# Kernel optimization log

Measured on AMD Instinct MI355X. Metric: run time of the kernel, lower is better.

## Reference

```python
import jax, jax.numpy as jnp
import numpy as np


def _conv1x1_relu(x, W, b):
    # x: (B, Cin, N, k), W: (Cout, Cin), b: (Cout,) -> (B, Cout, N, k)
    return jax.nn.relu(jnp.einsum('bcnk,oc->bonk', x, W) + b[None, :, None, None])


def _knn_idx(pc, k):
    # pc: (B, C, N). Mirrors torch: dis_mat = -||pi - pj||^2, topk (largest) -> nearest.
    G = jnp.einsum('bcn,bcm->bnm', pc, pc)            # (B, N, N)
    sq = jnp.sum(pc * pc, axis=1)                      # (B, N)
    neg_dist = 2.0 * G - sq[:, :, None] - sq[:, None, :]
    _, idx = jax.lax.top_k(neg_dist, k)                # (B, N, k) int32
    return idx


def _group_points(x, idx):
    # x: (B, C, N), idx: (B, N, k) -> (B, C, N, k); out[b,c,n,j] = x[b,c,idx[b,n,j]]
    B, C, N = x.shape
    k = idx.shape[-1]
    idx2 = jnp.broadcast_to(idx.reshape(B, 1, N * k), (B, C, N * k))
    return jnp.take_along_axis(x, idx2, axis=2).reshape(B, C, N, k)


def setup_inputs() -> dict:
    key = jax.random.key(0)
    ks = jax.random.split(key, 8)
    B, N, C, O, K = 8, 4096, 64, 64, 16
    s = 0.05
    return {
        'xyz': jax.random.normal(ks[0], (B, 3, N), dtype=jnp.float32),
        'fea': jax.random.normal(ks[1], (B, C, N), dtype=jnp.float32),
        'Wg1': jax.random.normal(ks[2], (O, 10), dtype=jnp.float32) * s,
        'bg1': jnp.zeros((O,), dtype=jnp.float32),
        'Wg2': jax.random.normal(ks[3], (O, O), dtype=jnp.float32) * s,
        'bg2': jnp.zeros((O,), dtype=jnp.float32),
        'Wf1': jax.random.normal(ks[4], (O, 2 * C), dtype=jnp.float32) * s,
        'bf1': jnp.zeros((O,), dtype=jnp.float32),
        'Wf2': jax.random.normal(ks[5], (O, O), dtype=jnp.float32) * s,
        'bf2': jnp.zeros((O,), dtype=jnp.float32),
        'Wf3': jax.random.normal(ks[6], (O, O), dtype=jnp.float32) * s,
        'bf3': jnp.zeros((O,), dtype=jnp.float32),
        'k': 16,
    }


def reference(xyz, fea, Wg1, bg1, Wg2, bg2, Wf1, bf1, Wf2, bf2, Wf3, bf3, k):
    idx = _knn_idx(fea, k)                             # (B, N, k)

    # get_edge_point: (B, 10, N, k)
    xyz_knn = _group_points(xyz, idx)                  # (B, 3, N, k)
    xyz_c = jnp.broadcast_to(xyz[:, :, :, None], xyz_knn.shape)
    xyz_r = xyz_c - xyz_knn
    xyz_d = jnp.sqrt(jnp.sum(xyz_r * xyz_r, axis=1, keepdims=True))
    geo = jnp.concatenate([xyz_d, xyz_c, xyz_knn, xyz_r], axis=1)

    # get_edge_feature: (B, 2C, N, k)
    fea_knn = _group_points(fea, idx)
    fea_c = jnp.broadcast_to(fea[:, :, :, None], fea_knn.shape)
    edge = jnp.concatenate([fea_c, fea_knn], axis=1)

    g = _conv1x1_relu(geo, Wg1, bg1)
    g = _conv1x1_relu(g, Wg2, bg2)

    f = _conv1x1_relu(edge, Wf1, bf1)
    f = _conv1x1_relu(f, Wf2, bf2)
    f = _conv1x1_relu(f, Wf3, bf3)

    out = jnp.max(g * f, axis=-1)                      # (B, O, N)
    return out
```

## Files before the change

### kernel.cpp

```cpp
#include <hip/hip_runtime.h>
#include <math.h>

#define NB 8
#define NPTS 4096
#define NCH 64
#define NOUT 64
#define KNN 16

#define GLOBAL_AS const __attribute__((address_space(1)))
#define LDS_AS __attribute__((address_space(3)))

#define WS_SQ  0
#define WS_PT  (NB*NPTS)
#define WS_QT  (WS_PT + NB*NPTS*64)
#define WS_IDX (WS_QT + NB*NPTS*64)

__global__ __launch_bounds__(256) void k_sq(const float* __restrict__ fea,
                                            float* __restrict__ sq) {
    int g = blockIdx.x * 256 + threadIdx.x;
    int b = g >> 12, n = g & 4095;
    const float* f = fea + (size_t)b * NCH * NPTS + n;
    float s = 0.f;
#pragma unroll
    for (int c = 0; c < NCH; ++c) s = fmaf(f[c * NPTS], f[c * NPTS], s);
    sq[g] = s;
}

__global__ __launch_bounds__(256, 4) void k_knn(const float* __restrict__ fea,
                                                const float* __restrict__ sq,
                                                int* __restrict__ idxout) {
    __shared__ __align__(16) float rowT[64][32];
    __shared__ __align__(16) float colT[2][64 * 64];

    const int b = blockIdx.y;
    const int n0 = blockIdx.x * 32;
    const int tid = threadIdx.x;
    const int lane = tid & 63, w = tid >> 6;
    const int g = lane >> 4, p = lane & 15;
    const int rbase = w * 8 + g * 2;
    const float* feab = fea + (size_t)b * NCH * NPTS;

    auto stage = [&](int buf, int m0) {
#pragma unroll
        for (int i = 0; i < 4; ++i) {
            int k = w * 4 + i;
            int c = 4 * k + (lane >> 4);
            int j = (lane & 15) * 4;
            const float* gp = feab + c * NPTS + m0 + j;
            float* lp = &colT[buf][k * 256];
            __builtin_amdgcn_global_load_lds((GLOBAL_AS void*)gp,
                                             (LDS_AS void*)lp, 16, 0, 0);
        }
    };

#pragma unroll
    for (int i = 0; i < 2; ++i) {
        int e = i * 1024 + tid * 4;
        int c = e >> 5, r = e & 31;
        *(float4*)&rowT[c][r] = *(const float4*)&feab[c * NPTS + n0 + r];
    }

    float lstv[2];
    int   lsti[2];
    float thr[2];
#pragma unroll
    for (int i = 0; i < 2; ++i) {
        lstv[i] = -3.0e38f; lsti[i] = 0; thr[i] = -3.0e38f;
    }

    auto ins = [&](int i, float vv, int col) {
        unsigned long long lt = __ballot(lstv[i] < vv);
        int pos = __popc((unsigned)((lt >> (g * 16)) & 0xFFFFu));
        int nv = __builtin_amdgcn_update_dpp(0, __float_as_int(lstv[i]),
                                             0x101, 0xF, 0xF, true);
        int ni = __builtin_amdgcn_update_dpp(0, lsti[i],
                                             0x101, 0xF, 0xF, true);
        if (p <= pos - 2)      { lstv[i] = __int_as_float(nv); lsti[i] = ni; }
        else if (p == pos - 1) { lstv[i] = vv; lsti[i] = col; }
    };

    stage(0, 0);
    __syncthreads();

    for (int t = 0; t < 64; ++t) {
        const int m0 = t * 64;
        const int cur = t & 1;
        if (t < 63) stage(cur ^ 1, m0 + 64);

        float4 sqc = *(const float4*)&sq[b * NPTS + m0 + p * 4];

        float acc[2][4] = {{0.f,0.f,0.f,0.f},{0.f,0.f,0.f,0.f}};
#pragma unroll 8
        for (int c = 0; c < 64; ++c) {
            float2 rv = *(const float2*)&rowT[c][rbase];
            float4 cv = *(const float4*)&colT[cur][c * 64 + p * 4];
            float cc[4] = {cv.x, cv.y, cv.z, cv.w};
#pragma unroll
            for (int ci = 0; ci < 4; ++ci) {
                acc[0][ci] = fmaf(rv.x, cc[ci], acc[0][ci]);
                acc[1][ci] = fmaf(rv.y, cc[ci], acc[1][ci]);
            }
        }

        float sqa[4] = {sqc.x, sqc.y, sqc.z, sqc.w};
#pragma unroll
        for (int i = 0; i < 2; ++i)
#pragma unroll
            for (int j = 0; j < 4; ++j)
                acc[i][j] = fmaf(2.f, acc[i][j], -sqa[j]);

#pragma unroll
        for (int i = 0; i < 2; ++i) {
            float v0 = acc[i][0], v1 = acc[i][1];
            float v2 = acc[i][2], v3 = acc[i][3];
            float vm = fmaxf(fmaxf(v0, v1), fmaxf(v2, v3));
            unsigned long long bal = __ballot(vm > thr[i]);
            unsigned mg = (unsigned)((bal >> (g * 16)) & 0xFFFFull);
            while (__any(mg != 0u)) {
                bool act = (mg != 0u);
                int srcp = act ? (__ffs(mg) - 1) : 0;
                mg &= (mg - 1u);
                int srcl = (g << 4) | srcp;
                float b0 = __shfl(v0, srcl);
                float b1 = __shfl(v1, srcl);
                float b2 = __shfl(v2, srcl);
                float b3 = __shfl(v3, srcl);
                if (act) {
                    int cb = m0 + srcp * 4;
                    if (b0 > thr[i]) ins(i, b0, cb + 0);
                    if (b1 > thr[i]) ins(i, b1, cb + 1);
                    if (b2 > thr[i]) ins(i, b2, cb + 2);
                    if (b3 > thr[i]) ins(i, b3, cb + 3);
                }
            }
            if (bal) thr[i] = __shfl(lstv[i], 0, 16);
        }
        __syncthreads();
    }

#pragma unroll
    for (int i = 0; i < 2; ++i) {
        int row = rbase + i;
        idxout[((size_t)(b * NPTS) + n0 + row) * KNN + (15 - p)] = lsti[i];
    }
}

__global__ __launch_bounds__(256) void k_pq(const float* __restrict__ fea,
                                            const float* __restrict__ Wf1,
                                            const float* __restrict__ bf1,
                                            float* __restrict__ Pt,
                                            float* __restrict__ Qt) {
    __shared__ __align__(16) float feaT[64][64];
    __shared__ __align__(16) float WT[64][132];
    __shared__ float sb[64];

    const int b = blockIdx.y;
    const int n0 = blockIdx.x * 64;
    const int tid = threadIdx.x;
    const int to = tid & 15, tn = tid >> 4;
    const float* feab = fea + (size_t)b * NCH * NPTS;

#pragma unroll
    for (int i = 0; i < 4; ++i) {
        int e = i * 1024 + tid * 4;
        int c = e >> 6, nn = e & 63;
        *(float4*)&feaT[c][nn] = *(const float4*)&feab[c * NPTS + n0 + nn];
    }
#pragma unroll
    for (int i = 0; i < 8; ++i) {
        int g = tid * 32 + i * 4;
        int op = g >> 6, c = g & 63;
        const float* src = (op < 64) ? &Wf1[op * 128 + c]
                                     : &Wf1[(op - 64) * 128 + 64 + c];
        float4 w = *(const float4*)src;
        WT[c + 0][op] = w.x; WT[c + 1][op] = w.y;
        WT[c + 2][op] = w.z; WT[c + 3][op] = w.w;
    }
    if (tid < 64) sb[tid] = bf1[tid];
    __syncthreads();

    float acc[4][8];
#pragma unroll
    for (int ni = 0; ni < 4; ++ni)
#pragma unroll
        for (int oj = 0; oj < 8; ++oj) acc[ni][oj] = 0.f;

#pragma unroll 4
    for (int c = 0; c < 64; ++c) {
        float4 a  = *(const float4*)&feaT[c][tn * 4];
        float4 w0 = *(const float4*)&WT[c][to * 8];
        float4 w1 = *(const float4*)&WT[c][to * 8 + 4];
        float av[4] = {a.x, a.y, a.z, a.w};
        float wv[8] = {w0.x, w0.y, w0.z, w0.w, w1.x, w1.y, w1.z, w1.w};
#pragma unroll
        for (int ni = 0; ni < 4; ++ni)
#pragma unroll
            for (int oj = 0; oj < 8; ++oj)
                acc[ni][oj] = fmaf(av[ni], wv[oj], acc[ni][oj]);
    }

    const int opb = to * 8;
#pragma unroll
    for (int ni = 0; ni < 4; ++ni) {
        int n = n0 + tn * 4 + ni;
        size_t base = ((size_t)b * NPTS + n) * 64;
        if (opb < 64) {
            float4 o0, o1;
            o0.x = acc[ni][0] + sb[opb + 0]; o0.y = acc[ni][1] + sb[opb + 1];
            o0.z = acc[ni][2] + sb[opb + 2]; o0.w = acc[ni][3] + sb[opb + 3];
            o1.x = acc[ni][4] + sb[opb + 4]; o1.y = acc[ni][5] + sb[opb + 5];
            o1.z = acc[ni][6] + sb[opb + 6]; o1.w = acc[ni][7] + sb[opb + 7];
            *(float4*)&Pt[base + opb]     = o0;
            *(float4*)&Pt[base + opb + 4] = o1;
        } else {
            float4 o0, o1;
            o0.x = acc[ni][0]; o0.y = acc[ni][1]; o0.z = acc[ni][2]; o0.w = acc[ni][3];
            o1.x = acc[ni][4]; o1.y = acc[ni][5]; o1.z = acc[ni][6]; o1.w = acc[ni][7];
            *(float4*)&Qt[base + opb - 64]     = o0;
            *(float4*)&Qt[base + opb - 64 + 4] = o1;
        }
    }
}

__global__ __launch_bounds__(256) void k_mlp(
    const float* __restrict__ xyz,
    const float* __restrict__ Pt, const float* __restrict__ Qt,
    const int* __restrict__ knnidx,
    const float* __restrict__ Wg1, const float* __restrict__ bg1,
    const float* __restrict__ Wg2, const float* __restrict__ bg2,
    const float* __restrict__ Wf2, const float* __restrict__ bf2,
    const float* __restrict__ Wf3, const float* __restrict__ bf3,
    float* __restrict__ out) {
    __shared__ __align__(16) float bufX[64][68];
    __shared__ __align__(16) float bufY[64][68];
    __shared__ __align__(16) float WbufA[64][68];
    __shared__ __align__(16) float WbufB[64][68];
    __shared__ __align__(16) float scratch[1280];
    __shared__ float biasA[64], biasB[64];
    __shared__ int sidx[64];

    const int b = blockIdx.y;
    const int n0 = blockIdx.x * 4;
    const int tid = threadIdx.x;
    const int to = tid & 15, tp = tid >> 4;

    if (tid < 64)
        sidx[tid] = knnidx[((size_t)(b * NPTS + n0)) * KNN + tid];
    __syncthreads();

    {
        int pair = tid >> 2, q = tid & 3;
        int blk = pair >> 2, sub = pair & 3;
        int m = sidx[pair];
        int pt = pair >> 4;
        const float* pB = &Pt[((size_t)b * NPTS + n0 + pt) * 64];
        const float* qB = &Qt[((size_t)b * NPTS + m) * 64];
#pragma unroll
        for (int i = 0; i < 4; ++i) {
            int c0 = q * 16 + i * 4;
            int f = ((q << 2) + i) & 7;
            int cp = 4 * (blk ^ f) + sub;
            float4 pv = *(const float4*)&pB[c0];
            float4 qv = *(const float4*)&qB[c0];
            bufX[c0 + 0][cp] = fmaxf(pv.x + qv.x, 0.f);
            bufX[c0 + 1][cp] = fmaxf(pv.y + qv.y, 0.f);
            bufX[c0 + 2][cp] = fmaxf(pv.z + qv.z, 0.f);
            bufX[c0 + 3][cp] = fmaxf(pv.w + qv.w, 0.f);
        }
    }
    if (tid < 64) {
        int pair = tid, pt = pair >> 4;
        int blk = pair >> 2, sub = pair & 3;
        int m = sidx[pair];
        const float* xb = xyz + (size_t)b * 3 * NPTS;
        float cx = xb[0 * NPTS + n0 + pt], cy = xb[1 * NPTS + n0 + pt], cz = xb[2 * NPTS + n0 + pt];
        float kx = xb[0 * NPTS + m], ky = xb[1 * NPTS + m], kz = xb[2 * NPTS + m];
        float rx = cx - kx, ry = cy - ky, rz = cz - kz;
        float d = sqrtf(rx * rx + ry * ry + rz * rz);
        float gv[10] = {d, cx, cy, cz, kx, ky, kz, rx, ry, rz};
#pragma unroll
        for (int ch = 0; ch < 10; ++ch) {
            int cp = 4 * (blk ^ ((ch >> 2) & 7)) + sub;
            scratch[ch * 68 + cp] = gv[ch];
        }
    }

    auto stageW = [&](const float* W, const float* bv, float (*Wb)[68],
                      float* bias) {
#pragma unroll
        for (int i = 0; i < 4; ++i) {
            int g = tid * 16 + i * 4;
            int o = g >> 6, c = g & 63;
            float4 w = *(const float4*)&W[g];
            Wb[c + 0][o] = w.x; Wb[c + 1][o] = w.y;
            Wb[c + 2][o] = w.z; Wb[c + 3][o] = w.w;
        }
        if (tid < 64) bias[tid] = bv[tid];
    };

    auto gemmPh = [&](const float* src, float* dst, int Kdim,
                      const float (*Wb)[68], const float* bias) {
        float acc[4][4] = {{0.f,0.f,0.f,0.f},{0.f,0.f,0.f,0.f},
                           {0.f,0.f,0.f,0.f},{0.f,0.f,0.f,0.f}};
#pragma unroll 2
        for (int c = 0; c < Kdim; ++c) {
            float4 w = *(const float4*)&Wb[c][to * 4];
            float4 a = *(const float4*)(src + c * 68 +
                                        4 * (tp ^ ((c >> 2) & 7)));
            float wr[4] = {w.x, w.y, w.z, w.w};
            float ar[4] = {a.x, a.y, a.z, a.w};
#pragma unroll
            for (int oi = 0; oi < 4; ++oi)
#pragma unroll
                for (int pj = 0; pj < 4; ++pj)
                    acc[oi][pj] = fmaf(wr[oi], ar[pj], acc[oi][pj]);
        }
#pragma unroll
        for (int oi = 0; oi < 4; ++oi) {
            int o = to * 4 + oi;
            float bo = bias[o];
            float4 o4;
            o4.x = fmaxf(acc[oi][0] + bo, 0.f);
            o4.y = fmaxf(acc[oi][1] + bo, 0.f);
            o4.z = fmaxf(acc[oi][2] + bo, 0.f);
            o4.w = fmaxf(acc[oi][3] + bo, 0.f);
            *(float4*)(dst + o * 68 + 4 * (tp ^ (to & 7))) = o4;
        }
    };

    stageW(Wf2, bf2, WbufA, biasA);
    stageW(Wf3, bf3, WbufB, biasB);
    __syncthreads();
    gemmPh(&bufX[0][0], &bufY[0][0], 64, WbufA, biasA);
    __syncthreads();
    gemmPh(&bufY[0][0], &bufX[0][0], 64, WbufB, biasB);
    {
        for (int e = tid; e < 640; e += 256) {
            int o = e / 10, c = e - o * 10;
            WbufA[c][o] = Wg1[e];
        }
        if (tid < 64) biasA[tid] = bg1[tid];
    }
    __syncthreads();
    gemmPh(scratch, &bufY[0][0], 10, WbufA, biasA);
    stageW(Wg2, bg2, WbufB, biasB);
    __syncthreads();
    {
        float acc[4][4] = {{0.f,0.f,0.f,0.f},{0.f,0.f,0.f,0.f},
                           {0.f,0.f,0.f,0.f},{0.f,0.f,0.f,0.f}};
#pragma unroll 2
        for (int c = 0; c < 64; ++c) {
            float4 w = *(const float4*)&WbufB[c][to * 4];
            float4 a = *(const float4*)&bufY[c][4 * (tp ^ ((c >> 2) & 7))];
            float wr[4] = {w.x, w.y, w.z, w.w};
            float ar[4] = {a.x, a.y, a.z, a.w};
#pragma unroll
            for (int oi = 0; oi < 4; ++oi)
#pragma unroll
                for (int pj = 0; pj < 4; ++pj)
                    acc[oi][pj] = fmaf(wr[oi], ar[pj], acc[oi][pj]);
        }
#pragma unroll
        for (int oi = 0; oi < 4; ++oi) {
            int o = to * 4 + oi;
            float bo = biasB[o];
            float4 f3q = *(const float4*)&bufX[o][4 * (tp ^ (to & 7))];
            float m0_ = fmaxf(acc[oi][0] + bo, 0.f) * f3q.x;
            float m1_ = fmaxf(acc[oi][1] + bo, 0.f) * f3q.y;
            float m2_ = fmaxf(acc[oi][2] + bo, 0.f) * f3q.z;
            float m3_ = fmaxf(acc[oi][3] + bo, 0.f) * f3q.w;
            scratch[o * 17 + tp] =
                fmaxf(fmaxf(m0_, m1_), fmaxf(m2_, m3_));
        }
    }
    __syncthreads();
    {
        int o = tid & 63, pt = tid >> 6;
        float m0_ = scratch[o * 17 + pt * 4 + 0];
        float m1  = scratch[o * 17 + pt * 4 + 1];
        float m2  = scratch[o * 17 + pt * 4 + 2];
        float m3  = scratch[o * 17 + pt * 4 + 3];
        out[((size_t)b * 64 + o) * NPTS + n0 + pt] =
            fmaxf(fmaxf(m0_, m1), fmaxf(m2, m3));
    }
}

extern "C" void kernel_launch(void* const* d_in, const int* in_sizes, int n_in,
                              void* d_out, int out_size, void* d_ws, size_t ws_size,
                              hipStream_t stream) {
    const float* xyz = (const float*)d_in[0];
    const float* fea = (const float*)d_in[1];
    const float* Wg1 = (const float*)d_in[2];
    const float* bg1 = (const float*)d_in[3];
    const float* Wg2 = (const float*)d_in[4];
    const float* bg2 = (const float*)d_in[5];
    const float* Wf1 = (const float*)d_in[6];
    const float* bf1 = (const float*)d_in[7];
    const float* Wf2 = (const float*)d_in[8];
    const float* bf2 = (const float*)d_in[9];
    const float* Wf3 = (const float*)d_in[10];
    const float* bf3 = (const float*)d_in[11];
    float* out = (float*)d_out;
    float* ws = (float*)d_ws;

    float* sq = ws + WS_SQ;
    float* Pt = ws + WS_PT;
    float* Qt = ws + WS_QT;
    int* idxw = (int*)(ws + WS_IDX);

    k_sq  <<<dim3(128),      dim3(256), 0, stream>>>(fea, sq);
    k_knn <<<dim3(128, 8),   dim3(256), 0, stream>>>(fea, sq, idxw);
    k_pq  <<<dim3(64, 8),    dim3(256), 0, stream>>>(fea, Wf1, bf1, Pt, Qt);
    k_mlp <<<dim3(1024, 8),  dim3(256), 0, stream>>>(xyz, Pt, Qt, idxw,
                                                     Wg1, bg1, Wg2, bg2,
                                                     Wf2, bf2, Wf3, bf3, out);
}
```

Baseline: 648.3 us.

## Batch four-candidate top-k insertion via rank merge and drop LDS swizzle

The KNN top-k maintenance replaces up to four sequential per-candidate insertions into the 16-lane sorted list with a single merge step. The merge computes each candidate's rank with four ballots and uses DPP shifts of 1 to 4 lanes to place the existing entries, which reduces the number of serial wave-level insert rounds. Separately, the fused MLP kernel drops its XOR swizzle on LDS columns and uses plain linear indexing. That simplifies address arithmetic but may reintroduce bank conflicts on the transposed stores.

```diff
diff --git a/kernel.cpp b/kernel.cpp
--- a/kernel.cpp
+++ b/kernel.cpp
@@ -68,15 +68,55 @@
         lstv[i] = -3.0e38f; lsti[i] = 0; thr[i] = -3.0e38f;
     }
 
-    auto ins = [&](int i, float vv, int col) {
-        unsigned long long lt = __ballot(lstv[i] < vv);
-        int pos = __popc((unsigned)((lt >> (g * 16)) & 0xFFFFu));
-        int nv = __builtin_amdgcn_update_dpp(0, __float_as_int(lstv[i]),
+    auto merge4 = [&](int i, bool act, float b0, float b1, float b2, float b3,
+                      int cb) {
+        const float NINF = -__builtin_inff();
+        float B0 = (act && b0 > thr[i]) ? b0 : NINF;
+        float B1 = (act && b1 > thr[i]) ? b1 : NINF;
+        float B2 = (act && b2 > thr[i]) ? b2 : NINF;
+        float B3 = (act && b3 > thr[i]) ? b3 : NINF;
+        int r0 = (B1 <= B0) + (B2 <= B0) + (B3 <= B0);
+        int r1 = (B0 <  B1) + (B2 <= B1) + (B3 <= B1);
+        int r2 = (B0 <  B2) + (B1 <  B2) + (B3 <= B2);
+        int r3 = (B0 <  B3) + (B1 <  B3) + (B2 <  B3);
+        unsigned long long t0 = __ballot(lstv[i] < B0);
+        unsigned long long t1 = __ballot(lstv[i] < B1);
+        unsigned long long t2 = __ballot(lstv[i] < B2);
+        unsigned long long t3 = __ballot(lstv[i] < B3);
+        const int sh = g * 16;
+        int rank0 = __popc((unsigned)((t0 >> sh) & 0xFFFFu)) + r0;
+        int rank1 = __popc((unsigned)((t1 >> sh) & 0xFFFFu)) + r1;
+        int rank2 = __popc((unsigned)((t2 >> sh) & 0xFFFFu)) + r2;
+        int rank3 = __popc((unsigned)((t3 >> sh) & 0xFFFFu)) + r3;
+        int cnt = (int)(B0 <= lstv[i]) + (int)(B1 <= lstv[i]) +
+                  (int)(B2 <= lstv[i]) + (int)(B3 <= lstv[i]);
+        int v1 = __builtin_amdgcn_update_dpp(0, __float_as_int(lstv[i]),
                                              0x101, 0xF, 0xF, true);
-        int ni = __builtin_amdgcn_update_dpp(0, lsti[i],
-                                             0x101, 0xF, 0xF, true);
-        if (p <= pos - 2)      { lstv[i] = __int_as_float(nv); lsti[i] = ni; }
-        else if (p == pos - 1) { lstv[i] = vv; lsti[i] = col; }
+        int i1 = __builtin_amdgcn_update_dpp(0, lsti[i], 0x101, 0xF, 0xF, true);
+        int c1 = __builtin_amdgcn_update_dpp(0, cnt,     0x101, 0xF, 0xF, true);
+        int v2 = __builtin_amdgcn_update_dpp(0, __float_as_int(lstv[i]),
+                                             0x102, 0xF, 0xF, true);
+        int i2 = __builtin_amdgcn_update_dpp(0, lsti[i], 0x102, 0xF, 0xF, true);
+        int c2 = __builtin_amdgcn_update_dpp(0, cnt,     0x102, 0xF, 0xF, true);
+        int v3 = __builtin_amdgcn_update_dpp(0, __float_as_int(lstv[i]),
+                                             0x103, 0xF, 0xF, true);
+        int i3 = __builtin_amdgcn_update_dpp(0, lsti[i], 0x103, 0xF, 0xF, true);
+        int c3 = __builtin_amdgcn_update_dpp(0, cnt,     0x103, 0xF, 0xF, true);
+        int v4 = __builtin_amdgcn_update_dpp(0, __float_as_int(lstv[i]),
+                                             0x104, 0xF, 0xF, true);
+        int i4 = __builtin_amdgcn_update_dpp(0, lsti[i], 0x104, 0xF, 0xF, true);
+        int c4 = __builtin_amdgcn_update_dpp(0, cnt,     0x104, 0xF, 0xF, true);
+        float nv = lstv[i]; int ni = lsti[i];
+        if (p <= 14 && c1 == 3) { nv = __int_as_float(v1); ni = i1; }
+        if (p <= 13 && c2 == 2) { nv = __int_as_float(v2); ni = i2; }
+        if (p <= 12 && c3 == 1) { nv = __int_as_float(v3); ni = i3; }
+        if (p <= 11 && c4 == 0) { nv = __int_as_float(v4); ni = i4; }
+        const int pr = p + 4;
+        if (rank0 == pr) { nv = B0; ni = cb + 0; }
+        if (rank1 == pr) { nv = B1; ni = cb + 1; }
+        if (rank2 == pr) { nv = B2; ni = cb + 2; }
+        if (rank3 == pr) { nv = B3; ni = cb + 3; }
+        lstv[i] = nv; lsti[i] = ni;
     };
 
     stage(0, 0);
@@ -125,13 +165,7 @@
                 float b1 = __shfl(v1, srcl);
                 float b2 = __shfl(v2, srcl);
                 float b3 = __shfl(v3, srcl);
-                if (act) {
-                    int cb = m0 + srcp * 4;
-                    if (b0 > thr[i]) ins(i, b0, cb + 0);
-                    if (b1 > thr[i]) ins(i, b1, cb + 1);
-                    if (b2 > thr[i]) ins(i, b2, cb + 2);
-                    if (b3 > thr[i]) ins(i, b3, cb + 3);
-                }
+                merge4(i, act, b0, b1, b2, b3, m0 + srcp * 4);
             }
             if (bal) thr[i] = __shfl(lstv[i], 0, 16);
         }
@@ -250,7 +284,6 @@
 
     {
         int pair = tid >> 2, q = tid & 3;
-        int blk = pair >> 2, sub = pair & 3;
         int m = sidx[pair];
         int pt = pair >> 4;
         const float* pB = &Pt[((size_t)b * NPTS + n0 + pt) * 64];
@@ -258,31 +291,26 @@
 #pragma unroll
         for (int i = 0; i < 4; ++i) {
             int c0 = q * 16 + i * 4;
-            int f = ((q << 2) + i) & 7;
-            int cp = 4 * (blk ^ f) + sub;
             float4 pv = *(const float4*)&pB[c0];
             float4 qv = *(const float4*)&qB[c0];
-            bufX[c0 + 0][cp] = fmaxf(pv.x + qv.x, 0.f);
-            bufX[c0 + 1][cp] = fmaxf(pv.y + qv.y, 0.f);
-            bufX[c0 + 2][cp] = fmaxf(pv.z + qv.z, 0.f);
-            bufX[c0 + 3][cp] = fmaxf(pv.w + qv.w, 0.f);
+            bufX[c0 + 0][pair] = fmaxf(pv.x + qv.x, 0.f);
+            bufX[c0 + 1][pair] = fmaxf(pv.y + qv.y, 0.f);
+            bufX[c0 + 2][pair] = fmaxf(pv.z + qv.z, 0.f);
+            bufX[c0 + 3][pair] = fmaxf(pv.w + qv.w, 0.f);
         }
     }
     if (tid < 64) {
         int pair = tid, pt = pair >> 4;
-        int blk = pair >> 2, sub = pair & 3;
         int m = sidx[pair];
         const float* xb = xyz + (size_t)b * 3 * NPTS;
         float cx = xb[0 * NPTS + n0 + pt], cy = xb[1 * NPTS + n0 + pt], cz = xb[2 * NPTS + n0 + pt];
         float kx = xb[0 * NPTS + m], ky = xb[1 * NPTS + m], kz = xb[2 * NPTS + m];
         float rx = cx - kx, ry = cy - ky, rz = cz - kz;
         float d = sqrtf(rx * rx + ry * ry + rz * rz);
-        float gv[10] = {d, cx, cy, cz, kx, ky, kz, rx, ry, rz};
-#pragma unroll
-        for (int ch = 0; ch < 10; ++ch) {
-            int cp = 4 * (blk ^ ((ch >> 2) & 7)) + sub;
-            scratch[ch * 68 + cp] = gv[ch];
-        }
+        scratch[0 * 68 + pair] = d;
+        scratch[1 * 68 + pair] = cx; scratch[2 * 68 + pair] = cy; scratch[3 * 68 + pair] = cz;
+        scratch[4 * 68 + pair] = kx; scratch[5 * 68 + pair] = ky; scratch[6 * 68 + pair] = kz;
+        scratch[7 * 68 + pair] = rx; scratch[8 * 68 + pair] = ry; scratch[9 * 68 + pair] = rz;
     }
 
     auto stageW = [&](const float* W, const float* bv, float (*Wb)[68],
@@ -305,8 +333,7 @@
 #pragma unroll 2
         for (int c = 0; c < Kdim; ++c) {
             float4 w = *(const float4*)&Wb[c][to * 4];
-            float4 a = *(const float4*)(src + c * 68 +
-                                        4 * (tp ^ ((c >> 2) & 7)));
+            float4 a = *(const float4*)(src + c * 68 + tp * 4);
             float wr[4] = {w.x, w.y, w.z, w.w};
             float ar[4] = {a.x, a.y, a.z, a.w};
 #pragma unroll
@@ -317,14 +344,13 @@
         }
 #pragma unroll
         for (int oi = 0; oi < 4; ++oi) {
-            int o = to * 4 + oi;
-            float bo = bias[o];
+            float bo = bias[to * 4 + oi];
             float4 o4;
             o4.x = fmaxf(acc[oi][0] + bo, 0.f);
             o4.y = fmaxf(acc[oi][1] + bo, 0.f);
             o4.z = fmaxf(acc[oi][2] + bo, 0.f);
             o4.w = fmaxf(acc[oi][3] + bo, 0.f);
-            *(float4*)(dst + o * 68 + 4 * (tp ^ (to & 7))) = o4;
+            *(float4*)(dst + (to * 4 + oi) * 68 + tp * 4) = o4;
         }
     };
 
@@ -351,7 +377,7 @@
 #pragma unroll 2
         for (int c = 0; c < 64; ++c) {
             float4 w = *(const float4*)&WbufB[c][to * 4];
-            float4 a = *(const float4*)&bufY[c][4 * (tp ^ ((c >> 2) & 7))];
+            float4 a = *(const float4*)&bufY[c][tp * 4];
             float wr[4] = {w.x, w.y, w.z, w.w};
             float ar[4] = {a.x, a.y, a.z, a.w};
 #pragma unroll
@@ -364,7 +390,7 @@
         for (int oi = 0; oi < 4; ++oi) {
             int o = to * 4 + oi;
             float bo = biasB[o];
-            float4 f3q = *(const float4*)&bufX[o][4 * (tp ^ (to & 7))];
+            float4 f3q = *(const float4*)&bufX[o][tp * 4];
             float m0_ = fmaxf(acc[oi][0] + bo, 0.f) * f3q.x;
             float m1_ = fmaxf(acc[oi][1] + bo, 0.f) * f3q.y;
             float m2_ = fmaxf(acc[oi][2] + bo, 0.f) * f3q.z;
```

New measurement: 734.6 us. 13.3% more time.
